# Optimization experiments

Hardware: AMD Instinct MI355X
Metric: run time of the kernel (lower is better)

## Reference

```python
import jax, jax.numpy as jnp
import numpy as np

B, N, F_IN, H, FO = 4, 2048, 256, 4, 64


def setup_inputs() -> dict:
    key = jax.random.key(0)
    k1, k2, k3, k4, k5 = jax.random.split(key, 5)
    x = jax.random.normal(k1, (B, N, F_IN), dtype=jnp.float32)
    # random 0/1 adjacency with self-loops so every row of softmax is finite
    adj = jax.random.randint(k2, (N, N), 0, 2).astype(jnp.float32)
    adj = jnp.maximum(adj, jnp.eye(N, dtype=jnp.float32))
    # parameters (xavier-uniform style)
    lim_w = float(np.sqrt(6.0 / (F_IN + H * FO)))
    W = jax.random.uniform(k3, (F_IN, H * FO), minval=-lim_w, maxval=lim_w, dtype=jnp.float32)
    lim_a = float(np.sqrt(6.0 / (H + FO)))
    a_src = jax.random.uniform(k4, (H, FO), minval=-lim_a, maxval=lim_a, dtype=jnp.float32)
    a_dst = jax.random.uniform(k5, (H, FO), minval=-lim_a, maxval=lim_a, dtype=jnp.float32)
    return {"x": x, "adj": adj, "W": W, "a_src": a_src, "a_dst": a_dst}


def reference(x, adj, W, a_src, a_dst):
    # h: (B, N, H, FO)
    h = (x @ W).reshape(B, N, H, FO)
    attn_src = jnp.einsum("bnhf,hf->bnh", h, a_src)  # (B,N,H)
    attn_dst = jnp.einsum("bnhf,hf->bnh", h, a_dst)  # (B,N,H)
    # scores[b,i,j,h] = src[b,i,h] + dst[b,j,h]
    scores = attn_src[:, :, None, :] + attn_dst[:, None, :, :]
    scores = jax.nn.leaky_relu(scores, negative_slope=0.2)
    mask = (adj == 0)[None, :, :, None]  # (1,N,N,1)
    scores = jnp.where(mask, -jnp.inf, scores)
    attn = jax.nn.softmax(scores, axis=2)  # softmax over neighbors j
    # dropout is identity in eval mode / p=0
    out = jnp.einsum("bijh,bjhf->bihf", attn, h)  # (B,N,H,FO)
    return out.reshape(B, N, H * FO)  # concat=True
```

## Files before the change

kernel.cpp:

```cpp
#include <hip/hip_runtime.h>
#include <hip/hip_bf16.h>
#include <math.h>

#define B 4
#define N 2048
#define FIN 256
#define H 4
#define FO 64
#define M (B*N)
#define HF (H*FO)

typedef __attribute__((ext_vector_type(8))) short short8;
typedef __attribute__((ext_vector_type(4))) float float4v;
typedef __attribute__((ext_vector_type(4))) int int4v;

#if __has_builtin(__builtin_amdgcn_exp2f)
#define EXP2(x) __builtin_amdgcn_exp2f(x)
#else
#define EXP2(x) exp2f(x)
#endif

static __device__ __forceinline__ unsigned int pk_rne(float a, float b) {
  unsigned int ua = __builtin_bit_cast(unsigned int, a);
  unsigned int ub = __builtin_bit_cast(unsigned int, b);
  ua += 0x7fffu + ((ua >> 16) & 1u);
  ub += 0x7fffu + ((ub >> 16) & 1u);
  return (ua >> 16) | (ub & 0xffff0000u);
}

static __device__ __forceinline__ unsigned int pk_trunc(float a, float b) {
#if __has_builtin(__builtin_amdgcn_perm)
  return __builtin_amdgcn_perm(__builtin_bit_cast(unsigned int, b),
                               __builtin_bit_cast(unsigned int, a), 0x07060302u);
#else
  return (__builtin_bit_cast(unsigned int, a) >> 16) |
         (__builtin_bit_cast(unsigned int, b) & 0xffff0000u);
#endif
}

static __device__ __forceinline__ void split_pair(float x0, float x1,
                                                  unsigned int& hi, unsigned int& lo) {
  unsigned int u0 = __builtin_bit_cast(unsigned int, x0);
  unsigned int u1 = __builtin_bit_cast(unsigned int, x1);
  hi = (u0 >> 16) | (u1 & 0xffff0000u);
  float h0 = __builtin_bit_cast(float, u0 & 0xffff0000u);
  float h1 = __builtin_bit_cast(float, u1 & 0xffff0000u);
  unsigned int l0 = __builtin_bit_cast(unsigned int, x0 - h0);
  unsigned int l1 = __builtin_bit_cast(unsigned int, x1 - h1);
  lo = (l0 >> 16) | (l1 & 0xffff0000u);
}

static __device__ __forceinline__ unsigned int fenc(float f) {
  unsigned int b = __builtin_bit_cast(unsigned int, f);
  return (b & 0x80000000u) ? ~b : (b | 0x80000000u);
}
static __device__ __forceinline__ float fdec(unsigned int e) {
  unsigned int b = (e & 0x80000000u) ? (e & 0x7fffffffu) : ~e;
  return __builtin_bit_cast(float, b);
}

__global__ __launch_bounds__(256) void prep_w(const float* __restrict__ Wsrc,
                                              unsigned short* __restrict__ Wt_hi,
                                              unsigned short* __restrict__ Wt_lo,
                                              unsigned int* __restrict__ DmaxEnc) {
  if (blockIdx.x == 0 && threadIdx.x < 16) DmaxEnc[threadIdx.x] = 0u;
  __shared__ float lds[64][65];
  const int k0 = (blockIdx.x >> 2) * 64;
  const int n0 = (blockIdx.x & 3) * 64;
  const int t = threadIdx.x;
  const int c4 = (t & 15) * 4;
  #pragma unroll
  for (int rep = 0; rep < 4; ++rep) {
    const int kl = (t >> 4) + 16 * rep;
    const float4 v = *(const float4*)(Wsrc + (size_t)(k0 + kl) * HF + n0 + c4);
    lds[kl][c4 + 0] = v.x; lds[kl][c4 + 1] = v.y;
    lds[kl][c4 + 2] = v.z; lds[kl][c4 + 3] = v.w;
  }
  __syncthreads();
  const int n  = t >> 2;
  const int kc = (t & 3) * 16;
  unsigned int hv[8], lv[8];
  #pragma unroll
  for (int p = 0; p < 8; ++p)
    split_pair(lds[kc + 2 * p][n], lds[kc + 2 * p + 1][n], hv[p], lv[p]);
  unsigned short* dh = Wt_hi + (size_t)(n0 + n) * FIN + k0 + kc;
  unsigned short* dl = Wt_lo + (size_t)(n0 + n) * FIN + k0 + kc;
  ((uint4*)dh)[0] = make_uint4(hv[0], hv[1], hv[2], hv[3]);
  ((uint4*)dh)[1] = make_uint4(hv[4], hv[5], hv[6], hv[7]);
  ((uint4*)dl)[0] = make_uint4(lv[0], lv[1], lv[2], lv[3]);
  ((uint4*)dl)[1] = make_uint4(lv[4], lv[5], lv[6], lv[7]);
}

__global__ __launch_bounds__(256) void pack_adj(const float* __restrict__ adj,
                                                unsigned long long* __restrict__ packed) {
  const int row = blockIdx.x;
  const int w = threadIdx.x >> 6, l = threadIdx.x & 63;
  const float* ar = adj + (size_t)row * N;
  for (int c = w; c < N / 64; c += 4) {
    unsigned long long m = __ballot(ar[c * 64 + l] != 0.f);
    if (l == 0) packed[(size_t)row * (N / 64) + c] = m;
  }
}

__global__ __launch_bounds__(256) void gemm_fused(const float* __restrict__ X,
                                                  const unsigned short* __restrict__ Wt_hi,
                                                  const unsigned short* __restrict__ Wt_lo,
                                                  const float* __restrict__ a_src,
                                                  const float* __restrict__ a_dst,
                                                  float* __restrict__ Srcv,
                                                  float2* __restrict__ Epair,
                                                  unsigned int* __restrict__ DmaxEnc,
                                                  unsigned short* __restrict__ Hf) {
  __shared__ unsigned short sh[64][72];
  __shared__ float smax[4];
  const int xcd  = blockIdx.x & 7;
  const int slot = blockIdx.x >> 3;
  const int mb = xcd * 16 + (slot >> 2);
  const int h  = slot & 3;
  const int w = threadIdx.x >> 6, lane = threadIdx.x & 63;
  const int fl = lane & 15, quad = lane >> 4, kk = quad * 8;
  const int m0 = mb * 64 + w * 16;
  const float* xr = X + (size_t)(m0 + fl) * FIN;
  const unsigned short* whb = Wt_hi + (size_t)(h * FO + fl) * FIN;
  const unsigned short* wlb = Wt_lo + (size_t)(h * FO + fl) * FIN;
  const float L2E = 1.4426950408889634f;

  const float4v zero = {0.f, 0.f, 0.f, 0.f};
  float4v acc[4] = {zero, zero, zero, zero};

  for (int k0 = 0; k0 < FIN; k0 += 32) {
    const float4 xa = *(const float4*)(xr + k0 + kk);
    const float4 xb = *(const float4*)(xr + k0 + kk + 4);
    const float xv[8] = {xa.x, xa.y, xa.z, xa.w, xb.x, xb.y, xb.z, xb.w};
    int hi[4], lo[4];
    #pragma unroll
    for (int p = 0; p < 4; ++p) {
      unsigned int hp, lp;
      split_pair(xv[2 * p], xv[2 * p + 1], hp, lp);
      hi[p] = (int)hp; lo[p] = (int)lp;
    }
    const short8 Ahi = __builtin_bit_cast(short8, (int4v){hi[0], hi[1], hi[2], hi[3]});
    const short8 Alo = __builtin_bit_cast(short8, (int4v){lo[0], lo[1], lo[2], lo[3]});
    #pragma unroll
    for (int t = 0; t < 4; ++t) {
      const short8 Bhi = *(const short8*)(whb + t * 16 * FIN + k0 + kk);
      const short8 Blo = *(const short8*)(wlb + t * 16 * FIN + k0 + kk);
      acc[t] = __builtin_amdgcn_mfma_f32_16x16x32_bf16(Ahi, Bhi, acc[t], 0, 0, 0);
      acc[t] = __builtin_amdgcn_mfma_f32_16x16x32_bf16(Alo, Bhi, acc[t], 0, 0, 0);
      acc[t] = __builtin_amdgcn_mfma_f32_16x16x32_bf16(Ahi, Blo, acc[t], 0, 0, 0);
    }
  }

  const int bb  = (mb * 64) >> 11;
  const int n0w = (mb * 64) & (N - 1);
  const int bh  = bb * H + h;
  float as[4], ad[4];
  #pragma unroll
  for (int t = 0; t < 4; ++t) {
    as[t] = a_src[h * FO + t * 16 + fl];
    ad[t] = a_dst[h * FO + t * 16 + fl];
  }
  float wmax = -INFINITY;
  #pragma unroll
  for (int reg = 0; reg < 4; ++reg) {
    float sv = 0.f, dv = 0.f;
    #pragma unroll
    for (int t = 0; t < 4; ++t) {
      sv = fmaf(acc[t][reg], as[t], sv);
      dv = fmaf(acc[t][reg], ad[t], dv);
    }
    #pragma unroll
    for (int off = 1; off <= 8; off <<= 1) {
      sv += __shfl_xor(sv, off, 64);
      dv += __shfl_xor(dv, off, 64);
    }
    wmax = fmaxf(wmax, dv);
    if (fl == 0) {
      const int node = n0w + w * 16 + quad * 4 + reg;
      Srcv[(bh << 11) + node] = sv;
      float2 e;
      e.x = EXP2(dv * L2E);
      e.y = EXP2(dv * (0.2f * L2E));
      Epair[(bh << 11) + node] = e;
    }
  }
  wmax = fmaxf(wmax, __shfl_xor(wmax, 16, 64));
  wmax = fmaxf(wmax, __shfl_xor(wmax, 32, 64));
  if (lane == 0) smax[w] = wmax;

  #pragma unroll
  for (int t = 0; t < 4; ++t) {
    const int nl = w * 16 + quad * 4;
    *(unsigned int*)&sh[t * 16 + fl][nl]     = pk_rne(acc[t][0], acc[t][1]);
    *(unsigned int*)&sh[t * 16 + fl][nl + 2] = pk_rne(acc[t][2], acc[t][3]);
  }
  __syncthreads();
  if (threadIdx.x == 0) {
    const float bmax = fmaxf(fmaxf(smax[0], smax[1]), fmaxf(smax[2], smax[3]));
    atomicMax(DmaxEnc + bh, fenc(bmax));
  }
  const int jc0 = n0w >> 5;
  #pragma unroll
  for (int rep = 0; rep < 2; ++rep) {
    const int s = (int)threadIdx.x + rep * 256;
    const int jcl = s >> 8;
    const int tt  = (s >> 6) & 3;
    const int ln  = s & 63;
    const int f    = tt * 16 + (ln & 15);
    const int node = jcl * 32 + (ln >> 4) * 8;
    unsigned short* dsth = Hf + (((size_t)bh * 64 + jc0 + jcl) * 4 + tt) * 512 + ln * 8;
    *(uint4*)dsth = *(const uint4*)&sh[f][node];
  }
}

__global__ __launch_bounds__(1024) void gat_mfma(const unsigned char* __restrict__ pb,
                                                 const float* __restrict__ Src,
                                                 const float2* __restrict__ Epair,
                                                 const unsigned int* __restrict__ DmaxEnc,
                                                 const unsigned short* __restrict__ Hf,
                                                 float* __restrict__ out) {
  const int xcd  = blockIdx.x & 7;
  const int slot = blockIdx.x >> 3;
  const int b    = xcd >> 1;
  const int i0   = ((xcd & 1) * 32 + slot) * 32;
  const int w    = threadIdx.x >> 6;
  const int lane = threadIdx.x & 63;
  const int h    = w & 3;
  const int q    = w >> 2;
  const int bh   = b * H + h;
  const int fl   = lane & 15;
  const int kk   = (lane >> 4) * 8;
  const float L2E = 1.4426950408889634f;

  const int row0 = i0 + fl;
  const int row1 = i0 + 16 + fl;
  const float dmx = fdec(DmaxEnc[bh]);
  const float s0 = Src[(bh << 11) + row0];
  const float s1 = Src[(bh << 11) + row1];
  const float u0 = s0 + dmx, m0 = fmaxf(u0, 0.2f * u0);
  const float u1 = s1 + dmx, m1 = fmaxf(u1, 0.2f * u1);
  const float c1a = EXP2((s0 - m0) * L2E), c2a = EXP2((0.2f * s0 - m0) * L2E);
  const float c1b = EXP2((s1 - m1) * L2E), c2b = EXP2((0.2f * s1 - m1) * L2E);
  const float ta = EXP2(-s0 * L2E), tb = EXP2(-s1 * L2E);
  const float* ep = (const float*)(Epair + (bh << 11));
  const unsigned char* pb0 = pb + (size_t)row0 * (N / 8);
  const unsigned char* pb1 = pb + (size_t)row1 * (N / 8);
  const unsigned short* hfb = Hf + (size_t)bh * 64 * 2048 + lane * 8;

  const short onebf = 0x3F80;
  short8 ones;
  #pragma unroll
  for (int jj = 0; jj < 8; ++jj) ones[jj] = onebf;

  const float4v zero = {0.f, 0.f, 0.f, 0.f};
  float4v acc[2][4];
  float4v accL[2];
  #pragma unroll
  for (int rt = 0; rt < 2; ++rt) {
    accL[rt] = zero;
    #pragma unroll
    for (int t = 0; t < 4; ++t) acc[rt][t] = zero;
  }

  const int jbeg = q * (N / 4);
  #pragma unroll 2
  for (int j0 = jbeg; j0 < jbeg + N / 4; j0 += 32) {
    const unsigned short* hc = hfb + (size_t)(j0 >> 5) * 2048;
    const short8 b0 = *(const short8*)(hc + 0 * 512);
    const short8 b1 = *(const short8*)(hc + 1 * 512);
    const short8 b2 = *(const short8*)(hc + 2 * 512);
    const short8 b3 = *(const short8*)(hc + 3 * 512);
    const float4 q0 = *(const float4*)(ep + 2 * (j0 + kk) + 0);
    const float4 q1 = *(const float4*)(ep + 2 * (j0 + kk) + 4);
    const float4 q2 = *(const float4*)(ep + 2 * (j0 + kk) + 8);
    const float4 q3 = *(const float4*)(ep + 2 * (j0 + kk) + 12);
    const unsigned int mk0 = pb0[(j0 + kk) >> 3];
    const unsigned int mk1 = pb1[(j0 + kk) >> 3];
    const float E1v[8] = {q0.x, q0.z, q1.x, q1.z, q2.x, q2.z, q3.x, q3.z};
    const float E2v[8] = {q0.y, q0.w, q1.y, q1.w, q2.y, q2.w, q3.y, q3.w};
    int p0i[4], p1i[4];
    #pragma unroll
    for (int p = 0; p < 4; ++p) {
      const int e0 = 2 * p, e1 = 2 * p + 1;
      const bool sa0 = E1v[e0] > ta;
      float va0 = (sa0 ? c1a : c2a) * (sa0 ? E1v[e0] : E2v[e0]);
      va0 = ((mk0 >> e0) & 1u) ? va0 : 0.f;
      const bool sa1 = E1v[e1] > ta;
      float va1 = (sa1 ? c1a : c2a) * (sa1 ? E1v[e1] : E2v[e1]);
      va1 = ((mk0 >> e1) & 1u) ? va1 : 0.f;
      p0i[p] = (int)pk_trunc(va0, va1);
      const bool sb0 = E1v[e0] > tb;
      float vb0 = (sb0 ? c1b : c2b) * (sb0 ? E1v[e0] : E2v[e0]);
      vb0 = ((mk1 >> e0) & 1u) ? vb0 : 0.f;
      const bool sb1 = E1v[e1] > tb;
      float vb1 = (sb1 ? c1b : c2b) * (sb1 ? E1v[e1] : E2v[e1]);
      vb1 = ((mk1 >> e1) & 1u) ? vb1 : 0.f;
      p1i[p] = (int)pk_trunc(vb0, vb1);
    }
    const short8 p0 = __builtin_bit_cast(short8, (int4v){p0i[0], p0i[1], p0i[2], p0i[3]});
    const short8 p1 = __builtin_bit_cast(short8, (int4v){p1i[0], p1i[1], p1i[2], p1i[3]});
    acc[0][0] = __builtin_amdgcn_mfma_f32_16x16x32_bf16(p0, b0, acc[0][0], 0, 0, 0);
    acc[0][1] = __builtin_amdgcn_mfma_f32_16x16x32_bf16(p0, b1, acc[0][1], 0, 0, 0);
    acc[0][2] = __builtin_amdgcn_mfma_f32_16x16x32_bf16(p0, b2, acc[0][2], 0, 0, 0);
    acc[0][3] = __builtin_amdgcn_mfma_f32_16x16x32_bf16(p0, b3, acc[0][3], 0, 0, 0);
    accL[0]   = __builtin_amdgcn_mfma_f32_16x16x32_bf16(p0, ones, accL[0], 0, 0, 0);
    acc[1][0] = __builtin_amdgcn_mfma_f32_16x16x32_bf16(p1, b0, acc[1][0], 0, 0, 0);
    acc[1][1] = __builtin_amdgcn_mfma_f32_16x16x32_bf16(p1, b1, acc[1][1], 0, 0, 0);
    acc[1][2] = __builtin_amdgcn_mfma_f32_16x16x32_bf16(p1, b2, acc[1][2], 0, 0, 0);
    acc[1][3] = __builtin_amdgcn_mfma_f32_16x16x32_bf16(p1, b3, acc[1][3], 0, 0, 0);
    accL[1]   = __builtin_amdgcn_mfma_f32_16x16x32_bf16(p1, ones, accL[1], 0, 0, 0);
  }

  __shared__ float4v parts[4][64][11];
  for (int r = 3; r >= 1; --r) {
    if (q == r) {
      #pragma unroll
      for (int rt = 0; rt < 2; ++rt) {
        #pragma unroll
        for (int t = 0; t < 4; ++t) parts[h][lane][rt * 5 + t] = acc[rt][t];
        parts[h][lane][rt * 5 + 4] = accL[rt];
      }
    }
    __syncthreads();
    if (q == r - 1) {
      #pragma unroll
      for (int rt = 0; rt < 2; ++rt) {
        #pragma unroll
        for (int t = 0; t < 4; ++t) acc[rt][t] += parts[h][lane][rt * 5 + t];
        accL[rt] += parts[h][lane][rt * 5 + 4];
      }
    }
    __syncthreads();
  }

  if (q == 0) {
    const int quad = lane >> 4;
    #pragma unroll
    for (int rt = 0; rt < 2; ++rt) {
      #pragma unroll
      for (int reg = 0; reg < 4; ++reg) {
        const int r = i0 + rt * 16 + quad * 4 + reg;
        const float invl = 1.f / accL[rt][reg];
        float* op = out + ((size_t)(b * N) + r) * HF + h * FO + fl;
        #pragma unroll
        for (int t = 0; t < 4; ++t) op[t * 16] = acc[rt][t][reg] * invl;
      }
    }
  }
}

extern "C" void kernel_launch(void* const* d_in, const int* in_sizes, int n_in,
                              void* d_out, int out_size, void* d_ws, size_t ws_size,
                              hipStream_t stream) {
  const float* x     = (const float*)d_in[0];
  const float* adj   = (const float*)d_in[1];
  const float* W     = (const float*)d_in[2];
  const float* a_src = (const float*)d_in[3];
  const float* a_dst = (const float*)d_in[4];
  float* out = (float*)d_out;

  char* p = (char*)d_ws;
  float* Srcv = (float*)p;                 p += (size_t)B * H * N * 4;
  float2* Epair = (float2*)p;              p += (size_t)B * H * N * 8;
  unsigned int* DmaxEnc = (unsigned int*)p; p += 256;
  unsigned short* Wth = (unsigned short*)p; p += (size_t)HF * FIN * 2;
  unsigned short* Wtl = (unsigned short*)p; p += (size_t)HF * FIN * 2;
  unsigned short* Hf  = (unsigned short*)p; p += (size_t)M * HF * 2;
  unsigned long long* packed = (unsigned long long*)p;

  prep_w<<<dim3(16), dim3(256), 0, stream>>>(W, Wth, Wtl, DmaxEnc);
  pack_adj<<<dim3(N), dim3(256), 0, stream>>>(adj, packed);
  gemm_fused<<<dim3((M / 64) * H), dim3(256), 0, stream>>>(x, Wth, Wtl, a_src, a_dst,
                                                           Srcv, Epair, DmaxEnc, Hf);
  gat_mfma<<<dim3(B * (N / 32)), dim3(1024), 0, stream>>>((const unsigned char*)packed,
                                                          Srcv, Epair, DmaxEnc, Hf, out);
}
```

Before: 141.3 us.

## Merge weight prep with adjacency packing and store W in MFMA fragment order

Combines the weight-split and adjacency-pack kernels into one launch, removing a launch boundary. Weight hi/lo bf16 parts are now stored in per-lane MFMA fragment order, so each wave's B-operand load is one contiguous 1 KB read instead of lane loads strided by a full row. This trades a more complex index mapping in the prep kernel for better-coalesced weight loads in the projection GEMM.

```diff
diff --git a/kernel.cpp b/kernel.cpp
--- a/kernel.cpp
+++ b/kernel.cpp
@@ -59,14 +59,27 @@
   return __builtin_bit_cast(float, b);
 }
 
-__global__ __launch_bounds__(256) void prep_w(const float* __restrict__ Wsrc,
-                                              unsigned short* __restrict__ Wt_hi,
-                                              unsigned short* __restrict__ Wt_lo,
-                                              unsigned int* __restrict__ DmaxEnc) {
+__global__ __launch_bounds__(256) void prep_pack(const float* __restrict__ Wsrc,
+                                                 const float* __restrict__ adj,
+                                                 unsigned short* __restrict__ Wf_hi,
+                                                 unsigned short* __restrict__ Wf_lo,
+                                                 unsigned long long* __restrict__ packed,
+                                                 unsigned int* __restrict__ DmaxEnc) {
+  if (blockIdx.x >= 16) {
+    const int row = blockIdx.x - 16;
+    const int w = threadIdx.x >> 6, l = threadIdx.x & 63;
+    const float* ar = adj + (size_t)row * N;
+    for (int c = w; c < N / 64; c += 4) {
+      unsigned long long m = __ballot(ar[c * 64 + l] != 0.f);
+      if (l == 0) packed[(size_t)row * (N / 64) + c] = m;
+    }
+    return;
+  }
   if (blockIdx.x == 0 && threadIdx.x < 16) DmaxEnc[threadIdx.x] = 0u;
   __shared__ float lds[64][65];
   const int k0 = (blockIdx.x >> 2) * 64;
-  const int n0 = (blockIdx.x & 3) * 64;
+  const int h  = blockIdx.x & 3;
+  const int n0 = h * 64;
   const int t = threadIdx.x;
   const int c4 = (t & 15) * 4;
   #pragma unroll
@@ -77,34 +90,27 @@
     lds[kl][c4 + 2] = v.z; lds[kl][c4 + 3] = v.w;
   }
   __syncthreads();
-  const int n  = t >> 2;
-  const int kc = (t & 3) * 16;
-  unsigned int hv[8], lv[8];
-  #pragma unroll
-  for (int p = 0; p < 8; ++p)
-    split_pair(lds[kc + 2 * p][n], lds[kc + 2 * p + 1][n], hv[p], lv[p]);
-  unsigned short* dh = Wt_hi + (size_t)(n0 + n) * FIN + k0 + kc;
-  unsigned short* dl = Wt_lo + (size_t)(n0 + n) * FIN + k0 + kc;
-  ((uint4*)dh)[0] = make_uint4(hv[0], hv[1], hv[2], hv[3]);
-  ((uint4*)dh)[1] = make_uint4(hv[4], hv[5], hv[6], hv[7]);
-  ((uint4*)dl)[0] = make_uint4(lv[0], lv[1], lv[2], lv[3]);
-  ((uint4*)dl)[1] = make_uint4(lv[4], lv[5], lv[6], lv[7]);
-}
-
-__global__ __launch_bounds__(256) void pack_adj(const float* __restrict__ adj,
-                                                unsigned long long* __restrict__ packed) {
-  const int row = blockIdx.x;
-  const int w = threadIdx.x >> 6, l = threadIdx.x & 63;
-  const float* ar = adj + (size_t)row * N;
-  for (int c = w; c < N / 64; c += 4) {
-    unsigned long long m = __ballot(ar[c * 64 + l] != 0.f);
-    if (l == 0) packed[(size_t)row * (N / 64) + c] = m;
+  #pragma unroll
+  for (int rep = 0; rep < 2; ++rep) {
+    const int s   = t + rep * 256;
+    const int kcl = s >> 8;
+    const int tt  = (s >> 6) & 3;
+    const int ln  = s & 63;
+    const int fL  = tt * 16 + (ln & 15);
+    const int kb  = kcl * 32 + (ln >> 4) * 8;
+    unsigned int hv[4], lv[4];
+    #pragma unroll
+    for (int p = 0; p < 4; ++p)
+      split_pair(lds[kb + 2 * p][fL], lds[kb + 2 * p + 1][fL], hv[p], lv[p]);
+    const size_t off = ((((size_t)h * 8 + (k0 >> 5) + kcl) * 4 + tt) << 9) + ln * 8;
+    *(uint4*)(Wf_hi + off) = make_uint4(hv[0], hv[1], hv[2], hv[3]);
+    *(uint4*)(Wf_lo + off) = make_uint4(lv[0], lv[1], lv[2], lv[3]);
   }
 }
 
 __global__ __launch_bounds__(256) void gemm_fused(const float* __restrict__ X,
-                                                  const unsigned short* __restrict__ Wt_hi,
-                                                  const unsigned short* __restrict__ Wt_lo,
+                                                  const unsigned short* __restrict__ Wf_hi,
+                                                  const unsigned short* __restrict__ Wf_lo,
                                                   const float* __restrict__ a_src,
                                                   const float* __restrict__ a_dst,
                                                   float* __restrict__ Srcv,
@@ -121,14 +127,13 @@
   const int fl = lane & 15, quad = lane >> 4, kk = quad * 8;
   const int m0 = mb * 64 + w * 16;
   const float* xr = X + (size_t)(m0 + fl) * FIN;
-  const unsigned short* whb = Wt_hi + (size_t)(h * FO + fl) * FIN;
-  const unsigned short* wlb = Wt_lo + (size_t)(h * FO + fl) * FIN;
   const float L2E = 1.4426950408889634f;
 
   const float4v zero = {0.f, 0.f, 0.f, 0.f};
   float4v acc[4] = {zero, zero, zero, zero};
 
   for (int k0 = 0; k0 < FIN; k0 += 32) {
+    const int kc = k0 >> 5;
     const float4 xa = *(const float4*)(xr + k0 + kk);
     const float4 xb = *(const float4*)(xr + k0 + kk + 4);
     const float xv[8] = {xa.x, xa.y, xa.z, xa.w, xb.x, xb.y, xb.z, xb.w};
@@ -143,8 +148,9 @@
     const short8 Alo = __builtin_bit_cast(short8, (int4v){lo[0], lo[1], lo[2], lo[3]});
     #pragma unroll
     for (int t = 0; t < 4; ++t) {
-      const short8 Bhi = *(const short8*)(whb + t * 16 * FIN + k0 + kk);
-      const short8 Blo = *(const short8*)(wlb + t * 16 * FIN + k0 + kk);
+      const size_t woff = ((((size_t)h * 8 + kc) * 4 + t) << 9) + lane * 8;
+      const short8 Bhi = *(const short8*)(Wf_hi + woff);
+      const short8 Blo = *(const short8*)(Wf_lo + woff);
       acc[t] = __builtin_amdgcn_mfma_f32_16x16x32_bf16(Ahi, Bhi, acc[t], 0, 0, 0);
       acc[t] = __builtin_amdgcn_mfma_f32_16x16x32_bf16(Alo, Bhi, acc[t], 0, 0, 0);
       acc[t] = __builtin_amdgcn_mfma_f32_16x16x32_bf16(Ahi, Blo, acc[t], 0, 0, 0);
@@ -363,14 +369,13 @@
   float* Srcv = (float*)p;                 p += (size_t)B * H * N * 4;
   float2* Epair = (float2*)p;              p += (size_t)B * H * N * 8;
   unsigned int* DmaxEnc = (unsigned int*)p; p += 256;
-  unsigned short* Wth = (unsigned short*)p; p += (size_t)HF * FIN * 2;
-  unsigned short* Wtl = (unsigned short*)p; p += (size_t)HF * FIN * 2;
+  unsigned short* Wfh = (unsigned short*)p; p += (size_t)HF * FIN * 2;
+  unsigned short* Wfl = (unsigned short*)p; p += (size_t)HF * FIN * 2;
   unsigned short* Hf  = (unsigned short*)p; p += (size_t)M * HF * 2;
   unsigned long long* packed = (unsigned long long*)p;
 
-  prep_w<<<dim3(16), dim3(256), 0, stream>>>(W, Wth, Wtl, DmaxEnc);
-  pack_adj<<<dim3(N), dim3(256), 0, stream>>>(adj, packed);
-  gemm_fused<<<dim3((M / 64) * H), dim3(256), 0, stream>>>(x, Wth, Wtl, a_src, a_dst,
+  prep_pack<<<dim3(16 + N), dim3(256), 0, stream>>>(W, adj, Wfh, Wfl, packed, DmaxEnc);
+  gemm_fused<<<dim3((M / 64) * H), dim3(256), 0, stream>>>(x, Wfh, Wfl, a_src, a_dst,
                                                            Srcv, Epair, DmaxEnc, Hf);
   gat_mfma<<<dim3(B * (N / 32)), dim3(1024), 0, stream>>>((const unsigned char*)packed,
                                                           Srcv, Epair, DmaxEnc, Hf, out);
```

Result: faster. 132.6 us (-6.1%).
